# Kernel tuning notes

Measured on AMD Instinct MI355X. Metric: run time of the kernel, lower is better.

## Reference

```python
import jax, jax.numpy as jnp
import numpy as np

B, H, I = 4096, 128, 128


def setup_inputs() -> dict:
    key = jax.random.key(0)
    ks = jax.random.split(key, 9)
    # xavier_uniform for W1/W2: fan_in = 2H*2I, fan_out = H*2I (torch treats dim0 as fan_out for >2D differently,
    # but we only need a plausible init; exact init values don't affect correctness of the math)
    def xavier(k, shape):
        fan_in = shape[1] * shape[2] if len(shape) == 3 else shape[0]
        fan_out = shape[0] * shape[2] if len(shape) == 3 else shape[1]
        lim = np.sqrt(6.0 / (fan_in + fan_out))
        return jax.random.uniform(k, shape, jnp.float32, -lim, lim)
    W1 = xavier(ks[0], (H, 2 * H, 2 * I))
    W2 = xavier(ks[1], (H, 2 * H, 2 * I))
    W3 = xavier(ks[2], (2 * H, H))
    fan_in, fan_out = 2 * H * 2 * I, H * 2 * I
    lim = float(np.sqrt(3.0 / (0.5 * (fan_in + fan_out))))
    b1 = jax.random.uniform(ks[3], (H,), jnp.float32, -lim, lim)
    b2 = jax.random.uniform(ks[4], (H,), jnp.float32, -lim, lim)
    in0 = jax.random.normal(ks[5], (B, I), jnp.float32)
    in1 = jax.random.normal(ks[6], (B, I), jnp.float32)
    st0 = jax.random.normal(ks[7], (B, H), jnp.float32)
    st1 = jax.random.normal(ks[8], (B, H), jnp.float32)
    return {"in0": in0, "in1": in1, "st0": st0, "st1": st1,
            "W1": W1, "b1": b1, "W2": W2, "b2": b2, "W3": W3}


def reference(in0, in1, st0, st1, W1, b1, W2, b2, W3):
    s = jnp.concatenate([st0, st1], axis=1)  # [B, 2H]
    x = jnp.concatenate([in0, in1], axis=1)  # [B, 2I]
    # Trilinear contraction; same math as outer-product-then-contract:
    # einsum('ij,ik->ijk') then ('ijk,ljk->il')  ==  'bj,bk,ljk->bl'
    m1 = jnp.einsum('bj,bk,ljk->bl', s, x, W1)  # [B, H]
    m2 = jnp.einsum('bj,bk,ljk->bl', s, x, W2)  # [B, H]
    u = jax.nn.sigmoid(m2 + b2)
    state_tilda = jnp.tanh(m1 + b1)
    new_state = u * state_tilda + (1.0 - u) * (s @ W3)
    return new_state
```

## Files before the change

kernel.cpp:

```cpp
#include <hip/hip_runtime.h>
#include <hip/hip_bf16.h>
#include <stdint.h>


typedef short bf8 __attribute__((ext_vector_type(8)));
typedef float f32x4 __attribute__((ext_vector_type(4)));

static constexpr size_t WT_OFF  = 0;
static constexpr size_t XBF_OFF = 33554432 + 2097152;
static constexpr size_t MP_OFF  = XBF_OFF + 2097152;

__device__ __forceinline__ unsigned f2bf(float f) {
    unsigned u = __builtin_bit_cast(unsigned, f);
    return (u + 0x7fffu + ((u >> 16) & 1u)) >> 16;
}
__device__ __forceinline__ unsigned pack2bf(float a, float b) {
    return f2bf(a) | (f2bf(b) << 16);
}

__global__ void prep_wx(const float* __restrict__ W1, const float* __restrict__ W2,
                        const float* __restrict__ in0, const float* __restrict__ in1,
                        uint4* __restrict__ Wt, unsigned* __restrict__ x_bf) {
    int bx = blockIdx.x;
    if (bx < 8192) {
        const int tid  = threadIdx.x;
        const int lane = tid & 63, wave = tid >> 6;
        const unsigned f = bx * 4 + wave;
        const unsigned n16 = f >> 11;
        const unsigned kchunk = (f >> 1) & 1023u;
        const unsigned kst = f & 1u;
        const unsigned n = n16 * 16 + (lane & 15);
        const unsigned K = kchunk * 64 + kst * 32 + (lane >> 4) * 8;
        const float* src = (n < 128 ? W1 + ((size_t)n << 16)
                                    : W2 + ((size_t)(n - 128) << 16)) + K;
        float4 a = ((const float4*)src)[0];
        float4 b = ((const float4*)src)[1];
        uint4 o;
        o.x = pack2bf(a.x, a.y); o.y = pack2bf(a.z, a.w);
        o.z = pack2bf(b.x, b.y); o.w = pack2bf(b.z, b.w);
        Wt[(size_t)f * 64 + lane] = o;
    } else {
        unsigned v = (bx - 8192) * 256 + threadIdx.x;
        unsigned b = v >> 6;
        unsigned j4 = (v & 63u) * 4u;
        const float* src = (j4 < 128) ? (in0 + (size_t)b * 128 + j4)
                                      : (in1 + (size_t)b * 128 + (j4 - 128));
        float4 a = *(const float4*)src;
        uint2 o;
        o.x = pack2bf(a.x, a.y);
        o.y = pack2bf(a.z, a.w);
        ((uint2*)x_bf)[v] = o;
    }
}

__launch_bounds__(256, 2)
__global__ void gemm_p(const unsigned char* __restrict__ Wt,
                       const float* __restrict__ st0, const float* __restrict__ st1,
                       const __hip_bfloat16* __restrict__ x_bf,
                       float* __restrict__ Mpart) {
    const int bx = blockIdx.x;
    const int ks = bx & 7;
    const int nt = (bx >> 3) & 1;
    const int mt = bx >> 4;
    const int b0 = mt << 7, n0 = nt << 7;
    const int tid  = threadIdx.x;
    const int lane = tid & 63, wave = tid >> 6;
    const int l15 = lane & 15, l4 = lane >> 4;

    __shared__ __align__(16) float Sl[32 * 132];
    for (int idx = tid; idx < 4096; idx += 256) {
        int r = idx >> 5, j = idx & 31;
        int jg = ks * 32 + j;
        float v = (jg < 128) ? st0[(size_t)(b0 + r) * 128 + jg]
                             : st1[(size_t)(b0 + r) * 128 + (jg - 128)];
        Sl[j * 132 + r] = v;
    }
    __syncthreads();

    const unsigned char* rbn[2];
    #pragma unroll
    for (int nf = 0; nf < 2; ++nf)
        rbn[nf] = Wt + ((size_t)(nt * 8 + wave * 2 + nf) << 21) + lane * 16;
    const float* sB = Sl + l4 * 4;

    f32x4 racc[8][2];
    #pragma unroll
    for (int mf = 0; mf < 8; ++mf)
        #pragma unroll
        for (int nf = 0; nf < 2; ++nf)
            racc[mf][nf] = (f32x4){0.f, 0.f, 0.f, 0.f};
    const f32x4 zacc = (f32x4){0.f, 0.f, 0.f, 0.f};

    auto kof = [&](int c) { return (size_t)(((ks * 32 + (c & 31)) * 4 + (c >> 5)) * 2048); };

    bf8 buf[2][2][2];
    #pragma unroll
    for (int nf = 0; nf < 2; ++nf)
        #pragma unroll
        for (int kst = 0; kst < 2; ++kst)
            buf[0][nf][kst] = *(const bf8*)(rbn[nf] + kof(0) + kst * 1024);

    bf8 a[8][2];

    #pragma unroll 2
    for (int c = 0; c < 128; ++c) {
        const int pp = c & 1;
        const int q = c >> 5, j = c & 31;
        if (j == 0) {
            const __hip_bfloat16* xb = x_bf + q * 64 + l4 * 8;
            #pragma unroll
            for (int mf = 0; mf < 8; ++mf)
                #pragma unroll
                for (int kst = 0; kst < 2; ++kst)
                    a[mf][kst] = *(const bf8*)(xb + (size_t)(b0 + mf * 16 + l15) * 256 + kst * 32);
        }
        {
            const size_t k1 = kof((c + 1) & 127);
            #pragma unroll
            for (int nf = 0; nf < 2; ++nf)
                #pragma unroll
                for (int kst = 0; kst < 2; ++kst)
                    buf[pp ^ 1][nf][kst] = *(const bf8*)(rbn[nf] + k1 + kst * 1024);
        }
        f32x4 sv[8];
        #pragma unroll
        for (int mf = 0; mf < 8; ++mf)
            sv[mf] = *(const f32x4*)(sB + j * 132 + mf * 16);
        #pragma unroll
        for (int nf = 0; nf < 2; ++nf) {
            bf8 bf0 = buf[pp][nf][0];
            bf8 bf1 = buf[pp][nf][1];
            #pragma unroll
            for (int mf = 0; mf < 8; ++mf) {
                f32x4 m0 = __builtin_amdgcn_mfma_f32_16x16x32_bf16(a[mf][0], bf0, zacc, 0, 0, 0);
                m0 = __builtin_amdgcn_mfma_f32_16x16x32_bf16(a[mf][1], bf1, m0, 0, 0, 0);
                racc[mf][nf] += sv[mf] * m0;
            }
        }
    }

    float* mp = Mpart + ((size_t)ks << 20);
    #pragma unroll
    for (int mf = 0; mf < 8; ++mf)
        #pragma unroll
        for (int nf = 0; nf < 2; ++nf) {
            int b = b0 + mf * 16 + l4 * 4;
            int n = n0 + wave * 32 + nf * 16 + l15;
            #pragma unroll
            for (int r = 0; r < 4; ++r)
                mp[(size_t)(b + r) * 256 + n] = racc[mf][nf][r];
        }
}

__global__ void epilogue(const float* __restrict__ st0, const float* __restrict__ st1,
                         const float* __restrict__ b1, const float* __restrict__ b2,
                         const float* __restrict__ W3, const float* __restrict__ Mpart,
                         float* __restrict__ out) {
    const int tid = threadIdx.x;
    const int h = tid & 127, rg = tid >> 7;
    const int bbase = blockIdx.x * 8;
    __shared__ float srow[8][256];
    #pragma unroll
    for (int i = 0; i < 8; ++i) {
        int idx = i * 256 + tid;
        int r = idx >> 8, j = idx & 255;
        float v = (j < 128) ? st0[(size_t)(bbase + r) * 128 + j]
                            : st1[(size_t)(bbase + r) * 128 + (j - 128)];
        srow[r][j] = v;
    }
    __syncthreads();
    float acc0 = 0.f, acc1 = 0.f, acc2 = 0.f, acc3 = 0.f;
    for (int j = 0; j < 256; ++j) {
        float w = W3[j * 128 + h];
        acc0 += srow[rg][j] * w;
        acc1 += srow[rg + 2][j] * w;
        acc2 += srow[rg + 4][j] * w;
        acc3 += srow[rg + 6][j] * w;
    }
    float accs[4] = {acc0, acc1, acc2, acc3};
    float bb1 = b1[h], bb2 = b2[h];
    #pragma unroll
    for (int i = 0; i < 4; ++i) {
        int b = bbase + rg + i * 2;
        float m1 = 0.f, m2 = 0.f;
        #pragma unroll
        for (int k = 0; k < 8; ++k) {
            m1 += Mpart[((size_t)k << 20) + (size_t)b * 256 + h];
            m2 += Mpart[((size_t)k << 20) + (size_t)b * 256 + 128 + h];
        }
        float u = 1.0f / (1.0f + expf(-(m2 + bb2)));
        float t = tanhf(m1 + bb1);
        out[(size_t)b * 128 + h] = u * t + (1.0f - u) * accs[i];
    }
}

extern "C" void kernel_launch(void* const* d_in, const int* in_sizes, int n_in,
                              void* d_out, int out_size, void* d_ws, size_t ws_size,
                              hipStream_t stream) {
    const float* in0 = (const float*)d_in[0];
    const float* in1 = (const float*)d_in[1];
    const float* st0 = (const float*)d_in[2];
    const float* st1 = (const float*)d_in[3];
    const float* W1  = (const float*)d_in[4];
    const float* b1  = (const float*)d_in[5];
    const float* W2  = (const float*)d_in[6];
    const float* b2  = (const float*)d_in[7];
    const float* W3  = (const float*)d_in[8];
    float* out = (float*)d_out;
    char* ws = (char*)d_ws;

    unsigned char* Wt   = (unsigned char*)(ws + WT_OFF);
    unsigned*      x_bf = (unsigned*)(ws + XBF_OFF);
    float*         Mp   = (float*)(ws + MP_OFF);

    prep_wx<<<9216, 256, 0, stream>>>(W1, W2, in0, in1, (uint4*)Wt, x_bf);
    gemm_p<<<512, 256, 0, stream>>>(Wt, st0, st1, (const __hip_bfloat16*)x_bf, Mp);
    epilogue<<<512, 256, 0, stream>>>(st0, st1, b1, b2, W3, Mp, out);
}
```

Before: 258.2 us.

## Switch trilinear GEMM to 32x32x16 MFMA with 2x2 wave tiling

The partial GEMM kernel now uses 32x32x16 bf16 MFMA tiles instead of 16x16x32. Waves are arranged in a 2x2 grid over a 128x128 output tile rather than each wave covering all rows. The weight pre-packing layout, the shared-memory state layout and the output store mapping are rewritten to match the 32x32 fragment format. The aim is fewer MFMA issues and less operand traffic per FLOP, since each wave now loads only its own 64 rows of x and its own B fragments. In exchange the per-element state scaling over 16-wide accumulators costs more VALU work and register pressure.

```diff
diff --git a/kernel.cpp b/kernel.cpp
--- a/kernel.cpp
+++ b/kernel.cpp
@@ -5,6 +5,7 @@
 
 typedef short bf8 __attribute__((ext_vector_type(8)));
 typedef float f32x4 __attribute__((ext_vector_type(4)));
+typedef float f32x16 __attribute__((ext_vector_type(16)));
 
 static constexpr size_t WT_OFF  = 0;
 static constexpr size_t XBF_OFF = 33554432 + 2097152;
@@ -26,11 +27,10 @@
         const int tid  = threadIdx.x;
         const int lane = tid & 63, wave = tid >> 6;
         const unsigned f = bx * 4 + wave;
-        const unsigned n16 = f >> 11;
-        const unsigned kchunk = (f >> 1) & 1023u;
-        const unsigned kst = f & 1u;
-        const unsigned n = n16 * 16 + (lane & 15);
-        const unsigned K = kchunk * 64 + kst * 32 + (lane >> 4) * 8;
+        const unsigned n5 = f >> 12;
+        const unsigned kc = f & 4095u;
+        const unsigned n = n5 * 32 + (lane & 31);
+        const unsigned K = kc * 16 + (lane >> 5) * 8;
         const float* src = (n < 128 ? W1 + ((size_t)n << 16)
                                     : W2 + ((size_t)(n - 128) << 16)) + K;
         float4 a = ((const float4*)src)[0];
@@ -60,95 +60,105 @@
                        float* __restrict__ Mpart) {
     const int bx = blockIdx.x;
     const int ks = bx & 7;
-    const int nt = (bx >> 3) & 1;
-    const int mt = bx >> 4;
-    const int b0 = mt << 7, n0 = nt << 7;
+    const int ntb = (bx >> 3) & 1;
+    const int mtb = bx >> 4;
+    const int b0 = mtb << 7, n0 = ntb << 7;
     const int tid  = threadIdx.x;
     const int lane = tid & 63, wave = tid >> 6;
-    const int l15 = lane & 15, l4 = lane >> 4;
-
-    __shared__ __align__(16) float Sl[32 * 132];
+    const int wm = wave & 1, wn = wave >> 1;
+    const int l31 = lane & 31, l5 = lane >> 5;
+
+    __shared__ __align__(16) float Sl2[32 * 132];
     for (int idx = tid; idx < 4096; idx += 256) {
-        int r = idx >> 5, j = idx & 31;
+        int j = idx >> 7, p = idx & 127;
+        int g = p >> 5, t = p & 31, h = t >> 4, r = t & 15;
+        int row = g * 32 + 4 * h + (r & 3) + 8 * (r >> 2);
         int jg = ks * 32 + j;
-        float v = (jg < 128) ? st0[(size_t)(b0 + r) * 128 + jg]
-                             : st1[(size_t)(b0 + r) * 128 + (jg - 128)];
-        Sl[j * 132 + r] = v;
+        float v = (jg < 128) ? st0[(size_t)(b0 + row) * 128 + jg]
+                             : st1[(size_t)(b0 + row) * 128 + (jg - 128)];
+        Sl2[j * 132 + p] = v;
     }
     __syncthreads();
 
     const unsigned char* rbn[2];
     #pragma unroll
-    for (int nf = 0; nf < 2; ++nf)
-        rbn[nf] = Wt + ((size_t)(nt * 8 + wave * 2 + nf) << 21) + lane * 16;
-    const float* sB = Sl + l4 * 4;
-
-    f32x4 racc[8][2];
-    #pragma unroll
-    for (int mf = 0; mf < 8; ++mf)
-        #pragma unroll
-        for (int nf = 0; nf < 2; ++nf)
-            racc[mf][nf] = (f32x4){0.f, 0.f, 0.f, 0.f};
-    const f32x4 zacc = (f32x4){0.f, 0.f, 0.f, 0.f};
-
-    auto kof = [&](int c) { return (size_t)(((ks * 32 + (c & 31)) * 4 + (c >> 5)) * 2048); };
-
-    bf8 buf[2][2][2];
-    #pragma unroll
-    for (int nf = 0; nf < 2; ++nf)
-        #pragma unroll
-        for (int kst = 0; kst < 2; ++kst)
-            buf[0][nf][kst] = *(const bf8*)(rbn[nf] + kof(0) + kst * 1024);
-
-    bf8 a[8][2];
+    for (int nt = 0; nt < 2; ++nt)
+        rbn[nt] = Wt + ((size_t)(ntb * 4 + wn * 2 + nt) << 22) + lane * 16;
+    const float* sB = Sl2 + wm * 64 + l5 * 16;
+
+    f32x16 racc[2][2];
+    #pragma unroll
+    for (int mt = 0; mt < 2; ++mt)
+        #pragma unroll
+        for (int nt = 0; nt < 2; ++nt)
+            racc[mt][nt] = (f32x16)(0.f);
+    const f32x16 zacc = (f32x16)(0.f);
+
+    auto kof = [&](int c) {
+        return (size_t)((((ks * 32 + (c & 31)) * 16) + (c >> 5) * 4) * 1024);
+    };
+
+    bf8 buf[2][2][4];
+    #pragma unroll
+    for (int nt = 0; nt < 2; ++nt)
+        #pragma unroll
+        for (int kf = 0; kf < 4; ++kf)
+            buf[0][nt][kf] = *(const bf8*)(rbn[nt] + kof(0) + kf * 1024);
+
+    bf8 a[2][4];
 
     #pragma unroll 2
     for (int c = 0; c < 128; ++c) {
         const int pp = c & 1;
         const int q = c >> 5, j = c & 31;
         if (j == 0) {
-            const __hip_bfloat16* xb = x_bf + q * 64 + l4 * 8;
-            #pragma unroll
-            for (int mf = 0; mf < 8; ++mf)
-                #pragma unroll
-                for (int kst = 0; kst < 2; ++kst)
-                    a[mf][kst] = *(const bf8*)(xb + (size_t)(b0 + mf * 16 + l15) * 256 + kst * 32);
+            const __hip_bfloat16* xb = x_bf + q * 64 + l5 * 8;
+            #pragma unroll
+            for (int mt = 0; mt < 2; ++mt)
+                #pragma unroll
+                for (int kf = 0; kf < 4; ++kf)
+                    a[mt][kf] = *(const bf8*)(xb + (size_t)(b0 + wm * 64 + mt * 32 + l31) * 256 + kf * 16);
         }
         {
             const size_t k1 = kof((c + 1) & 127);
             #pragma unroll
-            for (int nf = 0; nf < 2; ++nf)
-                #pragma unroll
-                for (int kst = 0; kst < 2; ++kst)
-                    buf[pp ^ 1][nf][kst] = *(const bf8*)(rbn[nf] + k1 + kst * 1024);
-        }
-        f32x4 sv[8];
-        #pragma unroll
-        for (int mf = 0; mf < 8; ++mf)
-            sv[mf] = *(const f32x4*)(sB + j * 132 + mf * 16);
-        #pragma unroll
-        for (int nf = 0; nf < 2; ++nf) {
-            bf8 bf0 = buf[pp][nf][0];
-            bf8 bf1 = buf[pp][nf][1];
-            #pragma unroll
-            for (int mf = 0; mf < 8; ++mf) {
-                f32x4 m0 = __builtin_amdgcn_mfma_f32_16x16x32_bf16(a[mf][0], bf0, zacc, 0, 0, 0);
-                m0 = __builtin_amdgcn_mfma_f32_16x16x32_bf16(a[mf][1], bf1, m0, 0, 0, 0);
-                racc[mf][nf] += sv[mf] * m0;
+            for (int nt = 0; nt < 2; ++nt)
+                #pragma unroll
+                for (int kf = 0; kf < 4; ++kf)
+                    buf[pp ^ 1][nt][kf] = *(const bf8*)(rbn[nt] + k1 + kf * 1024);
+        }
+        f32x4 sv4[2][4];
+        #pragma unroll
+        for (int mt = 0; mt < 2; ++mt)
+            #pragma unroll
+            for (int i = 0; i < 4; ++i)
+                sv4[mt][i] = *(const f32x4*)(sB + j * 132 + mt * 32 + i * 4);
+        #pragma unroll
+        for (int mt = 0; mt < 2; ++mt)
+            #pragma unroll
+            for (int nt = 0; nt < 2; ++nt) {
+                f32x16 m0 = zacc;
+                #pragma unroll
+                for (int kf = 0; kf < 4; ++kf)
+                    m0 = __builtin_amdgcn_mfma_f32_32x32x16_bf16(
+                        a[mt][kf], buf[pp][nt][kf], m0, 0, 0, 0);
+                #pragma unroll
+                for (int r = 0; r < 16; ++r)
+                    racc[mt][nt][r] += sv4[mt][r >> 2][r & 3] * m0[r];
             }
-        }
     }
 
     float* mp = Mpart + ((size_t)ks << 20);
     #pragma unroll
-    for (int mf = 0; mf < 8; ++mf)
-        #pragma unroll
-        for (int nf = 0; nf < 2; ++nf) {
-            int b = b0 + mf * 16 + l4 * 4;
-            int n = n0 + wave * 32 + nf * 16 + l15;
-            #pragma unroll
-            for (int r = 0; r < 4; ++r)
-                mp[(size_t)(b + r) * 256 + n] = racc[mf][nf][r];
+    for (int mt = 0; mt < 2; ++mt)
+        #pragma unroll
+        for (int nt = 0; nt < 2; ++nt) {
+            const int nn = n0 + wn * 64 + nt * 32 + l31;
+            #pragma unroll
+            for (int r = 0; r < 16; ++r) {
+                int b = b0 + wm * 64 + mt * 32 + (r & 3) + 8 * (r >> 2) + 4 * l5;
+                mp[(size_t)b * 256 + nn] = racc[mt][nt][r];
+            }
         }
 }
 
```

Result: slower. 269.4 us (+4.4%).

## Halve gemm N tile to 64 and double grid to 1024 blocks

Applied to the files above, without the earlier changes.

The per-block output tile in the trilinear GEMM shrinks from 128 to 64 columns. Each wave now handles one 16-column fragment instead of two, and the grid doubles to 1024 blocks. This gives more parallelism across the 256 CUs and cuts per-thread registers (accumulators and weight buffers), which can raise occupancy. In exchange, the A-operand (x) loads and the LDS state staging are repeated by twice as many blocks, and each weight load feeds half as many MFMAs per x fragment.

```diff
diff --git a/kernel.cpp b/kernel.cpp
--- a/kernel.cpp
+++ b/kernel.cpp
@@ -60,9 +60,9 @@
                        float* __restrict__ Mpart) {
     const int bx = blockIdx.x;
     const int ks = bx & 7;
-    const int nt = (bx >> 3) & 1;
-    const int mt = bx >> 4;
-    const int b0 = mt << 7, n0 = nt << 7;
+    const int ntq = (bx >> 3) & 3;
+    const int mt = bx >> 5;
+    const int b0 = mt << 7, n0 = ntq << 6;
     const int tid  = threadIdx.x;
     const int lane = tid & 63, wave = tid >> 6;
     const int l15 = lane & 15, l4 = lane >> 4;
@@ -77,28 +77,21 @@
     }
     __syncthreads();
 
-    const unsigned char* rbn[2];
-    #pragma unroll
-    for (int nf = 0; nf < 2; ++nf)
-        rbn[nf] = Wt + ((size_t)(nt * 8 + wave * 2 + nf) << 21) + lane * 16;
+    const unsigned char* rb = Wt + ((size_t)(ntq * 4 + wave) << 21) + lane * 16;
     const float* sB = Sl + l4 * 4;
 
-    f32x4 racc[8][2];
+    f32x4 racc[8];
     #pragma unroll
     for (int mf = 0; mf < 8; ++mf)
-        #pragma unroll
-        for (int nf = 0; nf < 2; ++nf)
-            racc[mf][nf] = (f32x4){0.f, 0.f, 0.f, 0.f};
+        racc[mf] = (f32x4){0.f, 0.f, 0.f, 0.f};
     const f32x4 zacc = (f32x4){0.f, 0.f, 0.f, 0.f};
 
     auto kof = [&](int c) { return (size_t)(((ks * 32 + (c & 31)) * 4 + (c >> 5)) * 2048); };
 
-    bf8 buf[2][2][2];
-    #pragma unroll
-    for (int nf = 0; nf < 2; ++nf)
-        #pragma unroll
-        for (int kst = 0; kst < 2; ++kst)
-            buf[0][nf][kst] = *(const bf8*)(rbn[nf] + kof(0) + kst * 1024);
+    bf8 buf[2][2];
+    #pragma unroll
+    for (int kst = 0; kst < 2; ++kst)
+        buf[0][kst] = *(const bf8*)(rb + kof(0) + kst * 1024);
 
     bf8 a[8][2];
 
@@ -117,39 +110,32 @@
         {
             const size_t k1 = kof((c + 1) & 127);
             #pragma unroll
-            for (int nf = 0; nf < 2; ++nf)
-                #pragma unroll
-                for (int kst = 0; kst < 2; ++kst)
-                    buf[pp ^ 1][nf][kst] = *(const bf8*)(rbn[nf] + k1 + kst * 1024);
+            for (int kst = 0; kst < 2; ++kst)
+                buf[pp ^ 1][kst] = *(const bf8*)(rb + k1 + kst * 1024);
         }
         f32x4 sv[8];
         #pragma unroll
         for (int mf = 0; mf < 8; ++mf)
             sv[mf] = *(const f32x4*)(sB + j * 132 + mf * 16);
-        #pragma unroll
-        for (int nf = 0; nf < 2; ++nf) {
-            bf8 bf0 = buf[pp][nf][0];
-            bf8 bf1 = buf[pp][nf][1];
-            #pragma unroll
-            for (int mf = 0; mf < 8; ++mf) {
-                f32x4 m0 = __builtin_amdgcn_mfma_f32_16x16x32_bf16(a[mf][0], bf0, zacc, 0, 0, 0);
-                m0 = __builtin_amdgcn_mfma_f32_16x16x32_bf16(a[mf][1], bf1, m0, 0, 0, 0);
-                racc[mf][nf] += sv[mf] * m0;
-            }
+        bf8 bf0 = buf[pp][0];
+        bf8 bf1 = buf[pp][1];
+        #pragma unroll
+        for (int mf = 0; mf < 8; ++mf) {
+            f32x4 m0 = __builtin_amdgcn_mfma_f32_16x16x32_bf16(a[mf][0], bf0, zacc, 0, 0, 0);
+            m0 = __builtin_amdgcn_mfma_f32_16x16x32_bf16(a[mf][1], bf1, m0, 0, 0, 0);
+            racc[mf] += sv[mf] * m0;
         }
     }
 
     float* mp = Mpart + ((size_t)ks << 20);
-    #pragma unroll
-    for (int mf = 0; mf < 8; ++mf)
-        #pragma unroll
-        for (int nf = 0; nf < 2; ++nf) {
-            int b = b0 + mf * 16 + l4 * 4;
-            int n = n0 + wave * 32 + nf * 16 + l15;
-            #pragma unroll
-            for (int r = 0; r < 4; ++r)
-                mp[(size_t)(b + r) * 256 + n] = racc[mf][nf][r];
-        }
+    const int nn = n0 + wave * 16 + l15;
+    #pragma unroll
+    for (int mf = 0; mf < 8; ++mf) {
+        int b = b0 + mf * 16 + l4 * 4;
+        #pragma unroll
+        for (int r = 0; r < 4; ++r)
+            mp[(size_t)(b + r) * 256 + nn] = racc[mf][r];
+    }
 }
 
 __global__ void epilogue(const float* __restrict__ st0, const float* __restrict__ st1,
@@ -214,6 +200,6 @@
     float*         Mp   = (float*)(ws + MP_OFF);
 
     prep_wx<<<9216, 256, 0, stream>>>(W1, W2, in0, in1, (uint4*)Wt, x_bf);
-    gemm_p<<<512, 256, 0, stream>>>(Wt, st0, st1, (const __hip_bfloat16*)x_bf, Mp);
+    gemm_p<<<1024, 256, 0, stream>>>(Wt, st0, st1, (const __hip_bfloat16*)x_bf, Mp);
     epilogue<<<512, 256, 0, stream>>>(st0, st1, b1, b2, W3, Mp, out);
 }
```

Result: slower. 285.0 us (+10.4%).
